# Performance work log

Measured on AMD Instinct MI355X. Metric: run time of the kernel, lower is better.

Reference implementation:

```python
import jax, jax.numpy as jnp
import numpy as np

N_NODES = 100000
EPS = 1e-12  # F.normalize eps


def _sage_conv(x, src, dst, deg, Wl, bl, Wr):
    # mean aggregation of neighbor (source) features at destination nodes
    agg = jax.ops.segment_sum(x[src], dst, num_segments=N_NODES)  # [N, F]
    agg = agg / jnp.maximum(deg, 1.0)[:, None]
    out = agg @ Wl + bl + x @ Wr  # lin_l(mean(x_j)) + lin_r(x_i)
    # normalize=True -> L2 row normalization
    norm = jnp.sqrt(jnp.sum(out * out, axis=-1, keepdims=True))
    return out / jnp.maximum(norm, EPS)


def setup_inputs() -> dict:
    key = jax.random.key(0)
    ks = jax.random.split(key, 10)
    F_IN, H, C = 14, 32, 2
    x = jax.random.normal(ks[0], (N_NODES, F_IN), dtype=jnp.float32)
    edge_index = jax.random.randint(ks[1], (2, 6400000), 0, N_NODES, dtype=jnp.int32)
    def glorot(k, shape):
        lim = float(np.sqrt(6.0 / (shape[0] + shape[1])))
        return jax.random.uniform(k, shape, jnp.float32, -lim, lim)
    return {
        "x": x,
        "edge_index": edge_index,
        "W1l": glorot(ks[2], (F_IN, H)), "b1": jnp.zeros((H,), jnp.float32),
        "W1r": glorot(ks[3], (F_IN, H)),
        "W2l": glorot(ks[4], (H, H)), "b2": jnp.zeros((H,), jnp.float32),
        "W2r": glorot(ks[5], (H, H)),
        "Wlin": glorot(ks[6], (H, C)), "blin": jnp.zeros((C,), jnp.float32),
    }


def reference(x, edge_index, W1l, b1, W1r, W2l, b2, W2r, Wlin, blin):
    src, dst = edge_index[0], edge_index[1]
    deg = jax.ops.segment_sum(jnp.ones_like(dst, dtype=x.dtype), dst,
                              num_segments=N_NODES)  # in-degree per node
    h = jax.nn.relu(_sage_conv(x, src, dst, deg, W1l, b1, W1r))
    # dropout p=0.2 is identity at inference
    h = jax.nn.relu(_sage_conv(h, src, dst, deg, W2l, b2, W2r))
    return h @ Wlin + blin  # [N, num_classes]
```

## Files before the change

### kernel.cpp

```cpp
#include <hip/hip_runtime.h>
#include <hip/hip_bf16.h>


#define CHA 16384
#define MAXB 512
#define CAPB 18432
#define NPB 128

static __device__ __forceinline__ unsigned short f2bf(float f) {
    unsigned u = __float_as_uint(f);
    unsigned r = (u + 0x7FFFu + ((u >> 16) & 1u)) >> 16;
    return (unsigned short)r;
}
#define BF_LO(u) __uint_as_float((u) << 16)
#define BF_HI(u) __uint_as_float((u) & 0xFFFF0000u)

__global__ void cvt_x_bf16(const float* __restrict__ x, unsigned short* __restrict__ xb,
                           int* __restrict__ bcursor, int N, int NB) {
    int idx = blockIdx.x * blockDim.x + threadIdx.x;
    if (idx < NB) bcursor[idx] = idx * CAPB;
    if (idx >= N * 16) return;
    int n = idx >> 4, f = idx & 15;
    float v = (f < 14) ? x[n * 14 + f] : 0.f;
    xb[idx] = f2bf(v);
}

__global__ __launch_bounds__(1024) void partitionA(
        const int* __restrict__ src, const int* __restrict__ dst,
        int* __restrict__ bcursor, unsigned* __restrict__ part, int E, int NB) {
    __shared__ unsigned pk[CHA];
    __shared__ int h[MAXB], lofs[MAXB], cur[MAXB], delta[MAXB], tmp[MAXB];
    int t = threadIdx.x;
    int base = blockIdx.x * CHA;
    int end = base + CHA; if (end > E) end = E;
    int cnt = end - base;

    int ed[16], es[16];
    for (int i = t; i < NB; i += 1024) h[i] = 0;
    __syncthreads();
    #pragma unroll
    for (int i = 0; i < 4; ++i) {
        int j = i * 4096 + t * 4;
        if (j + 4 <= cnt) {
            int4 d4 = *(const int4*)(dst + base + j);
            int4 s4 = *(const int4*)(src + base + j);
            ed[i*4+0] = d4.x; ed[i*4+1] = d4.y; ed[i*4+2] = d4.z; ed[i*4+3] = d4.w;
            es[i*4+0] = s4.x; es[i*4+1] = s4.y; es[i*4+2] = s4.z; es[i*4+3] = s4.w;
            atomicAdd(&h[d4.x >> 8], 1);
            atomicAdd(&h[d4.y >> 8], 1);
            atomicAdd(&h[d4.z >> 8], 1);
            atomicAdd(&h[d4.w >> 8], 1);
        } else {
            #pragma unroll
            for (int k = 0; k < 4; ++k) {
                if (j + k < cnt) {
                    ed[i*4+k] = dst[base + j + k];
                    es[i*4+k] = src[base + j + k];
                    atomicAdd(&h[ed[i*4+k] >> 8], 1);
                } else ed[i*4+k] = -1;
            }
        }
    }
    __syncthreads();
    int v = 0;
    if (t < MAXB) { v = (t < NB) ? h[t] : 0; tmp[t] = v; }
    __syncthreads();
    for (int off = 1; off < MAXB; off <<= 1) {
        int a = 0;
        if (t < MAXB && t >= off) a = tmp[t - off];
        __syncthreads();
        if (t < MAXB) tmp[t] += a;
        __syncthreads();
    }
    if (t < NB) {
        int excl = tmp[t] - v;
        lofs[t] = excl;
        cur[t] = excl;
        int g = v ? atomicAdd(&bcursor[t], v) : 0;
        delta[t] = g - excl;
    }
    __syncthreads();
    #pragma unroll
    for (int i = 0; i < 16; ++i) {
        int d = ed[i];
        if (d >= 0) {
            int b = d >> 8;
            int r = atomicAdd(&cur[b], 1);
            pk[r] = ((unsigned)(d & 255) << 24) | (unsigned)es[i];
        }
    }
    __syncthreads();
    int wid = t >> 6, lane = t & 63;
    for (int b = wid; b < NB; b += 16) {
        int s = lofs[b];
        int e2 = (b + 1 < NB) ? lofs[b + 1] : cnt;
        int dlt = delta[b];
        int lim = (b + 1) * CAPB;
        for (int k = s + lane; k < e2; k += 64) {
            int gidx = dlt + k;
            if (gidx < lim) part[gidx] = pk[k];
        }
    }
}

__global__ __launch_bounds__(1024) void partitionB(
        const unsigned* __restrict__ part, const int* __restrict__ bcursor,
        int* __restrict__ deg, int* __restrict__ offs, int* __restrict__ nlo,
        int* __restrict__ sorted_src, int N, int HALF) {
    __shared__ int pk2[CAPB];
    __shared__ int h[512], tmp[512], keyofs[512];
    int b = blockIdx.x;
    int t = threadIdx.x;
    int start = b * CAPB;
    int end = bcursor[b];
    if (end > start + CAPB) end = start + CAPB;
    int cnt = end - start;
    unsigned ce[18];
    if (t < 512) h[t] = 0;
    __syncthreads();
    #pragma unroll
    for (int i = 0; i < 18; ++i) {
        int idx = start + t + i * 1024;
        unsigned p = 0xFFFFFFFFu;
        if (idx < end) {
            p = part[idx];
            int key = (int)(p >> 24) * 2 + (((int)(p & 0xFFFFFFu) < HALF) ? 0 : 1);
            atomicAdd(&h[key], 1);
        }
        ce[i] = p;
    }
    __syncthreads();
    int v = (t < 512) ? h[t] : 0;
    if (t < 512) tmp[t] = v;
    __syncthreads();
    for (int off = 1; off < 512; off <<= 1) {
        int a = (t < 512 && t >= off) ? tmp[t - off] : 0;
        __syncthreads();
        if (t < 512) tmp[t] += a;
        __syncthreads();
    }
    if (t < 512) keyofs[t] = tmp[t] - v;
    __syncthreads();
    if (t < 256) {
        int lo = h[2 * t];
        int d = lo + h[2 * t + 1];
        int excl = keyofs[2 * t];
        int node = b * 256 + t;
        if (node < N) {
            deg[node] = d;
            offs[node] = start + excl;
            nlo[node] = lo;
        }
    }
    __syncthreads();
    #pragma unroll
    for (int i = 0; i < 18; ++i) {
        unsigned p = ce[i];
        if (p != 0xFFFFFFFFu) {
            int s = (int)(p & 0xFFFFFFu);
            int key = (int)(p >> 24) * 2 + ((s < HALF) ? 0 : 1);
            int r = atomicAdd(&keyofs[key], 1);
            pk2[r] = s;
        }
    }
    __syncthreads();
    for (int i = t; i < cnt; i += 1024)
        sorted_src[start + i] = pk2[i];
}

__global__ void gather14_bf16(const uint4* __restrict__ xb, const int* __restrict__ sorted_src,
                              const int* __restrict__ offs, const int* __restrict__ deg,
                              const int* __restrict__ nlo, float4* __restrict__ agg1,
                              int N, int pass) {
    int idx = blockIdx.x * blockDim.x + threadIdx.x;
    int n = idx >> 1;
    if (n >= N) return;
    int q = idx & 1;
    int start = offs[n];
    int d = deg[n];
    int lo = nlo[n];
    int jbeg = pass ? lo : 0;
    int jend = pass ? d : lo;
    float a0=0,a1=0,a2=0,a3=0,a4=0,a5=0,a6=0,a7=0;
    int j = jbeg;
    for (; j + 4 <= jend; j += 4) {
        int s0 = sorted_src[start + j + 0];
        int s1 = sorted_src[start + j + 1];
        int s2 = sorted_src[start + j + 2];
        int s3 = sorted_src[start + j + 3];
        uint4 u0 = xb[s0 * 2 + q];
        uint4 u1 = xb[s1 * 2 + q];
        uint4 u2 = xb[s2 * 2 + q];
        uint4 u3 = xb[s3 * 2 + q];
        a0 += BF_LO(u0.x) + BF_LO(u1.x) + BF_LO(u2.x) + BF_LO(u3.x);
        a1 += BF_HI(u0.x) + BF_HI(u1.x) + BF_HI(u2.x) + BF_HI(u3.x);
        a2 += BF_LO(u0.y) + BF_LO(u1.y) + BF_LO(u2.y) + BF_LO(u3.y);
        a3 += BF_HI(u0.y) + BF_HI(u1.y) + BF_HI(u2.y) + BF_HI(u3.y);
        a4 += BF_LO(u0.z) + BF_LO(u1.z) + BF_LO(u2.z) + BF_LO(u3.z);
        a5 += BF_HI(u0.z) + BF_HI(u1.z) + BF_HI(u2.z) + BF_HI(u3.z);
        a6 += BF_LO(u0.w) + BF_LO(u1.w) + BF_LO(u2.w) + BF_LO(u3.w);
        a7 += BF_HI(u0.w) + BF_HI(u1.w) + BF_HI(u2.w) + BF_HI(u3.w);
    }
    for (; j < jend; ++j) {
        uint4 u0 = xb[sorted_src[start + j] * 2 + q];
        a0 += BF_LO(u0.x); a1 += BF_HI(u0.x);
        a2 += BF_LO(u0.y); a3 += BF_HI(u0.y);
        a4 += BF_LO(u0.z); a5 += BF_HI(u0.z);
        a6 += BF_LO(u0.w); a7 += BF_HI(u0.w);
    }
    if (pass == 0) {
        agg1[n * 4 + q * 2 + 0] = make_float4(a0, a1, a2, a3);
        agg1[n * 4 + q * 2 + 1] = make_float4(a4, a5, a6, a7);
    } else {
        float inv = 1.0f / ((d > 0) ? (float)d : 1.0f);
        float4 p0 = agg1[n * 4 + q * 2 + 0];
        float4 p1 = agg1[n * 4 + q * 2 + 1];
        agg1[n * 4 + q * 2 + 0] = make_float4((p0.x + a0) * inv, (p0.y + a1) * inv,
                                              (p0.z + a2) * inv, (p0.w + a3) * inv);
        agg1[n * 4 + q * 2 + 1] = make_float4((p1.x + a4) * inv, (p1.y + a5) * inv,
                                              (p1.z + a6) * inv, (p1.w + a7) * inv);
    }
}

__global__ void gather32_bf16(const uint4* __restrict__ hb, const int* __restrict__ sorted_src,
                              const int* __restrict__ offs, const int* __restrict__ deg,
                              const int* __restrict__ nlo, float4* __restrict__ agg2,
                              int N, int pass) {
    int idx = blockIdx.x * blockDim.x + threadIdx.x;
    int n = idx >> 2;
    if (n >= N) return;
    int q = idx & 3;
    int start = offs[n];
    int d = deg[n];
    int lo = nlo[n];
    int jbeg = pass ? lo : 0;
    int jend = pass ? d : lo;
    float a0=0,a1=0,a2=0,a3=0,a4=0,a5=0,a6=0,a7=0;
    int j = jbeg;
    for (; j + 4 <= jend; j += 4) {
        int s0 = sorted_src[start + j + 0];
        int s1 = sorted_src[start + j + 1];
        int s2 = sorted_src[start + j + 2];
        int s3 = sorted_src[start + j + 3];
        uint4 u0 = hb[s0 * 4 + q];
        uint4 u1 = hb[s1 * 4 + q];
        uint4 u2 = hb[s2 * 4 + q];
        uint4 u3 = hb[s3 * 4 + q];
        a0 += BF_LO(u0.x) + BF_LO(u1.x) + BF_LO(u2.x) + BF_LO(u3.x);
        a1 += BF_HI(u0.x) + BF_HI(u1.x) + BF_HI(u2.x) + BF_HI(u3.x);
        a2 += BF_LO(u0.y) + BF_LO(u1.y) + BF_LO(u2.y) + BF_LO(u3.y);
        a3 += BF_HI(u0.y) + BF_HI(u1.y) + BF_HI(u2.y) + BF_HI(u3.y);
        a4 += BF_LO(u0.z) + BF_LO(u1.z) + BF_LO(u2.z) + BF_LO(u3.z);
        a5 += BF_HI(u0.z) + BF_HI(u1.z) + BF_HI(u2.z) + BF_HI(u3.z);
        a6 += BF_LO(u0.w) + BF_LO(u1.w) + BF_LO(u2.w) + BF_LO(u3.w);
        a7 += BF_HI(u0.w) + BF_HI(u1.w) + BF_HI(u2.w) + BF_HI(u3.w);
    }
    for (; j < jend; ++j) {
        uint4 u0 = hb[sorted_src[start + j] * 4 + q];
        a0 += BF_LO(u0.x); a1 += BF_HI(u0.x);
        a2 += BF_LO(u0.y); a3 += BF_HI(u0.y);
        a4 += BF_LO(u0.z); a5 += BF_HI(u0.z);
        a6 += BF_LO(u0.w); a7 += BF_HI(u0.w);
    }
    if (pass == 0) {
        agg2[n * 8 + q * 2 + 0] = make_float4(a0, a1, a2, a3);
        agg2[n * 8 + q * 2 + 1] = make_float4(a4, a5, a6, a7);
    } else {
        float inv = 1.0f / ((d > 0) ? (float)d : 1.0f);
        float4 p0 = agg2[n * 8 + q * 2 + 0];
        float4 p1 = agg2[n * 8 + q * 2 + 1];
        agg2[n * 8 + q * 2 + 0] = make_float4((p0.x + a0) * inv, (p0.y + a1) * inv,
                                              (p0.z + a2) * inv, (p0.w + a3) * inv);
        agg2[n * 8 + q * 2 + 1] = make_float4((p1.x + a4) * inv, (p1.y + a5) * inv,
                                              (p1.z + a6) * inv, (p1.w + a7) * inv);
    }
}

__global__ __launch_bounds__(256) void dense1(
        const float* __restrict__ x, const float* __restrict__ agg,
        const float* __restrict__ W1l, const float* __restrict__ b1,
        const float* __restrict__ W1r, float* __restrict__ h,
        unsigned short* __restrict__ hb, int N) {
    __shared__ float sagg[NPB * 17];
    __shared__ float sx[NPB * 15];
    __shared__ float swl[14 * 32], swr[14 * 32], sb[32];
    int t = threadIdx.x;
    int nb = blockIdx.x * NPB;
    int nn = N - nb; if (nn > NPB) nn = NPB;
    const float4* g4 = (const float4*)(agg + (size_t)nb * 16);
    for (int i = t; i < nn * 4; i += 256) {
        float4 v = g4[i];
        float* d = &sagg[(i >> 2) * 17 + (i & 3) * 4];
        d[0] = v.x; d[1] = v.y; d[2] = v.z; d[3] = v.w;
    }
    const float* gx = x + (size_t)nb * 14;
    for (int i = t; i < nn * 14; i += 256) {
        int row = i / 14;
        sx[row * 15 + (i - row * 14)] = gx[i];
    }
    for (int i = t; i < 448; i += 256) { swl[i] = W1l[i]; swr[i] = W1r[i]; }
    if (t < 32) sb[t] = b1[t];
    __syncthreads();
    int q2 = t & 3;
    int p = t >> 2;
    int l0 = p * 2, l1 = l0 + 1;
    float acc0[8], acc1[8];
    #pragma unroll
    for (int j = 0; j < 8; ++j) { acc0[j] = sb[q2 * 8 + j]; acc1[j] = acc0[j]; }
    #pragma unroll
    for (int k = 0; k < 14; ++k) {
        float a0 = sagg[l0 * 17 + k], a1 = sagg[l1 * 17 + k];
        float x0 = sx[l0 * 15 + k],  x1 = sx[l1 * 15 + k];
        const float4* wl4 = (const float4*)&swl[k * 32 + q2 * 8];
        const float4* wr4 = (const float4*)&swr[k * 32 + q2 * 8];
        float4 wla = wl4[0], wlb = wl4[1], wra = wr4[0], wrb = wr4[1];
        acc0[0] += a0 * wla.x + x0 * wra.x;  acc1[0] += a1 * wla.x + x1 * wra.x;
        acc0[1] += a0 * wla.y + x0 * wra.y;  acc1[1] += a1 * wla.y + x1 * wra.y;
        acc0[2] += a0 * wla.z + x0 * wra.z;  acc1[2] += a1 * wla.z + x1 * wra.z;
        acc0[3] += a0 * wla.w + x0 * wra.w;  acc1[3] += a1 * wla.w + x1 * wra.w;
        acc0[4] += a0 * wlb.x + x0 * wrb.x;  acc1[4] += a1 * wlb.x + x1 * wrb.x;
        acc0[5] += a0 * wlb.y + x0 * wrb.y;  acc1[5] += a1 * wlb.y + x1 * wrb.y;
        acc0[6] += a0 * wlb.z + x0 * wrb.z;  acc1[6] += a1 * wlb.z + x1 * wrb.z;
        acc0[7] += a0 * wlb.w + x0 * wrb.w;  acc1[7] += a1 * wlb.w + x1 * wrb.w;
    }
    float ss0 = 0.f, ss1 = 0.f;
    #pragma unroll
    for (int j = 0; j < 8; ++j) { ss0 += acc0[j] * acc0[j]; ss1 += acc1[j] * acc1[j]; }
    ss0 += __shfl_xor(ss0, 1); ss0 += __shfl_xor(ss0, 2);
    ss1 += __shfl_xor(ss1, 1); ss1 += __shfl_xor(ss1, 2);
    float inv0 = 1.f / fmaxf(sqrtf(ss0), 1e-12f);
    float inv1 = 1.f / fmaxf(sqrtf(ss1), 1e-12f);
    int n0 = nb + l0, n1 = nb + l1;
    if (n0 < N) {
        float hv[8];
        #pragma unroll
        for (int j = 0; j < 8; ++j) hv[j] = fmaxf(acc0[j] * inv0, 0.f);
        float4* ho = (float4*)(h + (size_t)n0 * 32);
        ho[q2 * 2 + 0] = make_float4(hv[0], hv[1], hv[2], hv[3]);
        ho[q2 * 2 + 1] = make_float4(hv[4], hv[5], hv[6], hv[7]);
        uint4 pb;
        pb.x = (unsigned)f2bf(hv[0]) | ((unsigned)f2bf(hv[1]) << 16);
        pb.y = (unsigned)f2bf(hv[2]) | ((unsigned)f2bf(hv[3]) << 16);
        pb.z = (unsigned)f2bf(hv[4]) | ((unsigned)f2bf(hv[5]) << 16);
        pb.w = (unsigned)f2bf(hv[6]) | ((unsigned)f2bf(hv[7]) << 16);
        ((uint4*)(hb + (size_t)n0 * 32))[q2] = pb;
    }
    if (n1 < N) {
        float hv[8];
        #pragma unroll
        for (int j = 0; j < 8; ++j) hv[j] = fmaxf(acc1[j] * inv1, 0.f);
        float4* ho = (float4*)(h + (size_t)n1 * 32);
        ho[q2 * 2 + 0] = make_float4(hv[0], hv[1], hv[2], hv[3]);
        ho[q2 * 2 + 1] = make_float4(hv[4], hv[5], hv[6], hv[7]);
        uint4 pb;
        pb.x = (unsigned)f2bf(hv[0]) | ((unsigned)f2bf(hv[1]) << 16);
        pb.y = (unsigned)f2bf(hv[2]) | ((unsigned)f2bf(hv[3]) << 16);
        pb.z = (unsigned)f2bf(hv[4]) | ((unsigned)f2bf(hv[5]) << 16);
        pb.w = (unsigned)f2bf(hv[6]) | ((unsigned)f2bf(hv[7]) << 16);
        ((uint4*)(hb + (size_t)n1 * 32))[q2] = pb;
    }
}

__global__ __launch_bounds__(256) void dense2(
        const float* __restrict__ h, const float* __restrict__ agg2,
        const float* __restrict__ W2l, const float* __restrict__ b2,
        const float* __restrict__ W2r, const float* __restrict__ Wlin,
        const float* __restrict__ blin, float* __restrict__ out, int N) {
    __shared__ float sa[NPB * 33];
    __shared__ float sh2[NPB * 33];
    __shared__ float swl[32 * 32], swr[32 * 32], swo[64], sb[32], sbo[2];
    int t = threadIdx.x;
    int nb = blockIdx.x * NPB;
    int nn = N - nb; if (nn > NPB) nn = NPB;
    const float4* ga = (const float4*)(agg2 + (size_t)nb * 32);
    const float4* gh = (const float4*)(h + (size_t)nb * 32);
    for (int i = t; i < nn * 8; i += 256) {
        float4 v = ga[i];
        float* d = &sa[(i >> 3) * 33 + (i & 7) * 4];
        d[0] = v.x; d[1] = v.y; d[2] = v.z; d[3] = v.w;
        float4 w = gh[i];
        float* e = &sh2[(i >> 3) * 33 + (i & 7) * 4];
        e[0] = w.x; e[1] = w.y; e[2] = w.z; e[3] = w.w;
    }
    for (int i = t; i < 1024; i += 256) { swl[i] = W2l[i]; swr[i] = W2r[i]; }
    if (t < 64) swo[t] = Wlin[t];
    if (t < 32) sb[t] = b2[t];
    if (t < 2) sbo[t] = blin[t];
    __syncthreads();
    int q2 = t & 3;
    int p = t >> 2;
    int l0 = p * 2, l1 = l0 + 1;
    float acc0[8], acc1[8];
    #pragma unroll
    for (int j = 0; j < 8; ++j) { acc0[j] = sb[q2 * 8 + j]; acc1[j] = acc0[j]; }
    for (int k = 0; k < 32; ++k) {
        float a0 = sa[l0 * 33 + k],  a1 = sa[l1 * 33 + k];
        float h0 = sh2[l0 * 33 + k], h1 = sh2[l1 * 33 + k];
        const float4* wl4 = (const float4*)&swl[k * 32 + q2 * 8];
        const float4* wr4 = (const float4*)&swr[k * 32 + q2 * 8];
        float4 wla = wl4[0], wlb = wl4[1], wra = wr4[0], wrb = wr4[1];
        acc0[0] += a0 * wla.x + h0 * wra.x;  acc1[0] += a1 * wla.x + h1 * wra.x;
        acc0[1] += a0 * wla.y + h0 * wra.y;  acc1[1] += a1 * wla.y + h1 * wra.y;
        acc0[2] += a0 * wla.z + h0 * wra.z;  acc1[2] += a1 * wla.z + h1 * wra.z;
        acc0[3] += a0 * wla.w + h0 * wra.w;  acc1[3] += a1 * wla.w + h1 * wra.w;
        acc0[4] += a0 * wlb.x + h0 * wrb.x;  acc1[4] += a1 * wlb.x + h1 * wrb.x;
        acc0[5] += a0 * wlb.y + h0 * wrb.y;  acc1[5] += a1 * wlb.y + h1 * wrb.y;
        acc0[6] += a0 * wlb.z + h0 * wrb.z;  acc1[6] += a1 * wlb.z + h1 * wrb.z;
        acc0[7] += a0 * wlb.w + h0 * wrb.w;  acc1[7] += a1 * wlb.w + h1 * wrb.w;
    }
    float ss0 = 0.f, ss1 = 0.f;
    #pragma unroll
    for (int j = 0; j < 8; ++j) { ss0 += acc0[j] * acc0[j]; ss1 += acc1[j] * acc1[j]; }
    ss0 += __shfl_xor(ss0, 1); ss0 += __shfl_xor(ss0, 2);
    ss1 += __shfl_xor(ss1, 1); ss1 += __shfl_xor(ss1, 2);
    float inv0 = 1.f / fmaxf(sqrtf(ss0), 1e-12f);
    float inv1 = 1.f / fmaxf(sqrtf(ss1), 1e-12f);
    float o00 = 0.f, o01 = 0.f, o10 = 0.f, o11 = 0.f;
    #pragma unroll
    for (int j = 0; j < 8; ++j) {
        float hv0 = fmaxf(acc0[j] * inv0, 0.f);
        float hv1 = fmaxf(acc1[j] * inv1, 0.f);
        int kk = q2 * 8 + j;
        o00 += hv0 * swo[kk * 2 + 0];
        o01 += hv0 * swo[kk * 2 + 1];
        o10 += hv1 * swo[kk * 2 + 0];
        o11 += hv1 * swo[kk * 2 + 1];
    }
    o00 += __shfl_xor(o00, 1); o00 += __shfl_xor(o00, 2);
    o01 += __shfl_xor(o01, 1); o01 += __shfl_xor(o01, 2);
    o10 += __shfl_xor(o10, 1); o10 += __shfl_xor(o10, 2);
    o11 += __shfl_xor(o11, 1); o11 += __shfl_xor(o11, 2);
    if (q2 == 0) {
        int n0 = nb + l0, n1 = nb + l1;
        if (n0 < N) { out[n0 * 2 + 0] = o00 + sbo[0]; out[n0 * 2 + 1] = o01 + sbo[1]; }
        if (n1 < N) { out[n1 * 2 + 0] = o10 + sbo[0]; out[n1 * 2 + 1] = o11 + sbo[1]; }
    }
}

extern "C" void kernel_launch(void* const* d_in, const int* in_sizes, int n_in,
                              void* d_out, int out_size, void* d_ws, size_t ws_size,
                              hipStream_t stream) {
    const float* x    = (const float*)d_in[0];
    const int*   ei   = (const int*)d_in[1];
    const float* W1l  = (const float*)d_in[2];
    const float* b1   = (const float*)d_in[3];
    const float* W1r  = (const float*)d_in[4];
    const float* W2l  = (const float*)d_in[5];
    const float* b2   = (const float*)d_in[6];
    const float* W2r  = (const float*)d_in[7];
    const float* Wlin = (const float*)d_in[8];
    const float* blin = (const float*)d_in[9];
    float* out = (float*)d_out;

    const int N = in_sizes[0] / 14;
    const int E = in_sizes[1] / 2;
    const int* src = ei;
    const int* dst = ei + E;
    const int NB = (N + 255) / 256;
    const int HALF = N / 2;

    char* ws = (char*)d_ws;
    size_t off = 0;
    auto alloc = [&](size_t bytes) -> void* {
        void* p = ws + off;
        off = (off + bytes + 255) & ~(size_t)255;
        return p;
    };
    int*            bcursor    = (int*)alloc((size_t)NB * 4);
    unsigned*       part       = (unsigned*)alloc((size_t)NB * CAPB * 4);
    int*            sorted_src = (int*)alloc((size_t)NB * CAPB * 4);
    int*            deg        = (int*)alloc((size_t)N * 4);
    int*            offs       = (int*)alloc((size_t)N * 4);
    int*            nlo        = (int*)alloc((size_t)N * 4);
    unsigned short* xb         = (unsigned short*)alloc((size_t)N * 16 * 2);
    float*          agg1       = (float*)alloc((size_t)N * 16 * 4);
    float*          hbuf       = (float*)alloc((size_t)N * 32 * 4);
    unsigned short* hb         = (unsigned short*)alloc((size_t)N * 32 * 2);
    float*          agg2       = (float*)part;
    (void)ws_size; (void)n_in; (void)out_size;

    cvt_x_bf16<<<(N * 16 + 255) / 256, 256, 0, stream>>>(x, xb, bcursor, N, NB);
    partitionA<<<(E + CHA - 1) / CHA, 1024, 0, stream>>>(src, dst, bcursor, part, E, NB);
    partitionB<<<NB, 1024, 0, stream>>>(part, bcursor, deg, offs, nlo, sorted_src, N, HALF);

    const int DB = (N + NPB - 1) / NPB;
    gather14_bf16<<<(N * 2 + 255) / 256, 256, 0, stream>>>(
        (const uint4*)xb, sorted_src, offs, deg, nlo, (float4*)agg1, N, 0);
    gather14_bf16<<<(N * 2 + 255) / 256, 256, 0, stream>>>(
        (const uint4*)xb, sorted_src, offs, deg, nlo, (float4*)agg1, N, 1);
    dense1<<<DB, 256, 0, stream>>>(x, agg1, W1l, b1, W1r, hbuf, hb, N);
    gather32_bf16<<<(N * 4 + 255) / 256, 256, 0, stream>>>(
        (const uint4*)hb, sorted_src, offs, deg, nlo, (float4*)agg2, N, 0);
    gather32_bf16<<<(N * 4 + 255) / 256, 256, 0, stream>>>(
        (const uint4*)hb, sorted_src, offs, deg, nlo, (float4*)agg2, N, 1);
    dense2<<<DB, 256, 0, stream>>>(hbuf, agg2, W2l, b2, W2r, Wlin, blin, out, N);
}
```

Baseline: 295.4 us.

## Fuse layer-1 gather and dense into partition kernel; fuse layer-2 pass1 with dense2

Layer-1 aggregation now runs inside the per-bucket partition kernel, reading neighbor indices straight from shared memory, then applies the first dense layer, normalization and bf16 packing before writing h. The second pass of the layer-2 gather is merged with dense2, so each thread computes partial 32-wide products and reduces them with shuffles. This drops the agg1 buffer and four separate launches along with their global round trips. In exchange, the partition kernel uses more shared memory and registers, which can lower occupancy, and dense2 keeps 32 accumulators per thread.

```diff
diff --git a/kernel.cpp b/kernel.cpp
--- a/kernel.cpp
+++ b/kernel.cpp
@@ -5,7 +5,6 @@
 #define CHA 16384
 #define MAXB 512
 #define CAPB 18432
-#define NPB 128
 
 static __device__ __forceinline__ unsigned short f2bf(float f) {
     unsigned u = __float_as_uint(f);
@@ -103,12 +102,20 @@
     }
 }
 
-__global__ __launch_bounds__(1024) void partitionB(
+__global__ __launch_bounds__(1024) void partitionB_fused(
         const unsigned* __restrict__ part, const int* __restrict__ bcursor,
+        const uint4* __restrict__ xb4, const float* __restrict__ x,
+        const float* __restrict__ W1l, const float* __restrict__ b1,
+        const float* __restrict__ W1r,
         int* __restrict__ deg, int* __restrict__ offs, int* __restrict__ nlo,
-        int* __restrict__ sorted_src, int N, int HALF) {
+        int* __restrict__ sorted_src, float* __restrict__ hbuf,
+        unsigned short* __restrict__ hb, int N, int HALF) {
     __shared__ int pk2[CAPB];
-    __shared__ int h[512], tmp[512], keyofs[512];
+    __shared__ int hh[512], tmp[512], keyofs[512];
+    __shared__ int lstart[256], ldeg[256];
+    __shared__ float sagg[256 * 17];
+    __shared__ float sx[256 * 14];
+    __shared__ float swl[448], swr[448], sb1[32];
     int b = blockIdx.x;
     int t = threadIdx.x;
     int start = b * CAPB;
@@ -116,7 +123,9 @@
     if (end > start + CAPB) end = start + CAPB;
     int cnt = end - start;
     unsigned ce[18];
-    if (t < 512) h[t] = 0;
+    if (t < 512) hh[t] = 0;
+    if (t < 448) { swl[t] = W1l[t]; swr[t] = W1r[t]; }
+    else if (t < 480) sb1[t - 448] = b1[t - 448];
     __syncthreads();
     #pragma unroll
     for (int i = 0; i < 18; ++i) {
@@ -125,26 +134,33 @@
         if (idx < end) {
             p = part[idx];
             int key = (int)(p >> 24) * 2 + (((int)(p & 0xFFFFFFu) < HALF) ? 0 : 1);
-            atomicAdd(&h[key], 1);
+            atomicAdd(&hh[key], 1);
         }
         ce[i] = p;
     }
-    __syncthreads();
-    int v = (t < 512) ? h[t] : 0;
+    {
+        int nnod = N - b * 256; if (nnod > 256) nnod = 256; if (nnod < 0) nnod = 0;
+        const float* gx = x + (size_t)b * 256 * 14;
+        for (int i = t; i < nnod * 14; i += 1024) sx[i] = gx[i];
+    }
+    __syncthreads();
+    int v = (t < 512) ? hh[t] : 0;
     if (t < 512) tmp[t] = v;
     __syncthreads();
     for (int off = 1; off < 512; off <<= 1) {
-        int a = (t < 512 && t >= off) ? tmp[t - off] : 0;
+        int a2 = (t < 512 && t >= off) ? tmp[t - off] : 0;
         __syncthreads();
-        if (t < 512) tmp[t] += a;
+        if (t < 512) tmp[t] += a2;
         __syncthreads();
     }
     if (t < 512) keyofs[t] = tmp[t] - v;
     __syncthreads();
     if (t < 256) {
-        int lo = h[2 * t];
-        int d = lo + h[2 * t + 1];
+        int lo = hh[2 * t];
+        int d = lo + hh[2 * t + 1];
         int excl = keyofs[2 * t];
+        lstart[t] = excl;
+        ldeg[t] = d;
         int node = b * 256 + t;
         if (node < N) {
             deg[node] = d;
@@ -166,77 +182,92 @@
     __syncthreads();
     for (int i = t; i < cnt; i += 1024)
         sorted_src[start + i] = pk2[i];
-}
-
-__global__ void gather14_bf16(const uint4* __restrict__ xb, const int* __restrict__ sorted_src,
-                              const int* __restrict__ offs, const int* __restrict__ deg,
-                              const int* __restrict__ nlo, float4* __restrict__ agg1,
-                              int N, int pass) {
-    int idx = blockIdx.x * blockDim.x + threadIdx.x;
-    int n = idx >> 1;
-    if (n >= N) return;
-    int q = idx & 1;
-    int start = offs[n];
-    int d = deg[n];
-    int lo = nlo[n];
-    int jbeg = pass ? lo : 0;
-    int jend = pass ? d : lo;
-    float a0=0,a1=0,a2=0,a3=0,a4=0,a5=0,a6=0,a7=0;
-    int j = jbeg;
-    for (; j + 4 <= jend; j += 4) {
-        int s0 = sorted_src[start + j + 0];
-        int s1 = sorted_src[start + j + 1];
-        int s2 = sorted_src[start + j + 2];
-        int s3 = sorted_src[start + j + 3];
-        uint4 u0 = xb[s0 * 2 + q];
-        uint4 u1 = xb[s1 * 2 + q];
-        uint4 u2 = xb[s2 * 2 + q];
-        uint4 u3 = xb[s3 * 2 + q];
-        a0 += BF_LO(u0.x) + BF_LO(u1.x) + BF_LO(u2.x) + BF_LO(u3.x);
-        a1 += BF_HI(u0.x) + BF_HI(u1.x) + BF_HI(u2.x) + BF_HI(u3.x);
-        a2 += BF_LO(u0.y) + BF_LO(u1.y) + BF_LO(u2.y) + BF_LO(u3.y);
-        a3 += BF_HI(u0.y) + BF_HI(u1.y) + BF_HI(u2.y) + BF_HI(u3.y);
-        a4 += BF_LO(u0.z) + BF_LO(u1.z) + BF_LO(u2.z) + BF_LO(u3.z);
-        a5 += BF_HI(u0.z) + BF_HI(u1.z) + BF_HI(u2.z) + BF_HI(u3.z);
-        a6 += BF_LO(u0.w) + BF_LO(u1.w) + BF_LO(u2.w) + BF_LO(u3.w);
-        a7 += BF_HI(u0.w) + BF_HI(u1.w) + BF_HI(u2.w) + BF_HI(u3.w);
-    }
-    for (; j < jend; ++j) {
-        uint4 u0 = xb[sorted_src[start + j] * 2 + q];
-        a0 += BF_LO(u0.x); a1 += BF_HI(u0.x);
-        a2 += BF_LO(u0.y); a3 += BF_HI(u0.y);
-        a4 += BF_LO(u0.z); a5 += BF_HI(u0.z);
-        a6 += BF_LO(u0.w); a7 += BF_HI(u0.w);
-    }
-    if (pass == 0) {
-        agg1[n * 4 + q * 2 + 0] = make_float4(a0, a1, a2, a3);
-        agg1[n * 4 + q * 2 + 1] = make_float4(a4, a5, a6, a7);
-    } else {
-        float inv = 1.0f / ((d > 0) ? (float)d : 1.0f);
-        float4 p0 = agg1[n * 4 + q * 2 + 0];
-        float4 p1 = agg1[n * 4 + q * 2 + 1];
-        agg1[n * 4 + q * 2 + 0] = make_float4((p0.x + a0) * inv, (p0.y + a1) * inv,
-                                              (p0.z + a2) * inv, (p0.w + a3) * inv);
-        agg1[n * 4 + q * 2 + 1] = make_float4((p1.x + a4) * inv, (p1.y + a5) * inv,
-                                              (p1.z + a6) * inv, (p1.w + a7) * inv);
-    }
-}
-
-__global__ void gather32_bf16(const uint4* __restrict__ hb, const int* __restrict__ sorted_src,
-                              const int* __restrict__ offs, const int* __restrict__ deg,
-                              const int* __restrict__ nlo, float4* __restrict__ agg2,
-                              int N, int pass) {
+
+    int node = t >> 2, sub = t & 3, ep = sub >> 1, half = sub & 1;
+    int js = lstart[node], d = ldeg[node];
+    int je = js + d;
+    float a[8] = {0,0,0,0,0,0,0,0};
+    int j = js + ep;
+    for (; j + 6 < je; j += 8) {
+        int s0 = pk2[j], s1 = pk2[j+2], s2 = pk2[j+4], s3 = pk2[j+6];
+        uint4 u0 = xb4[s0*2+half], u1 = xb4[s1*2+half], u2 = xb4[s2*2+half], u3 = xb4[s3*2+half];
+        a[0] += BF_LO(u0.x)+BF_LO(u1.x)+BF_LO(u2.x)+BF_LO(u3.x);
+        a[1] += BF_HI(u0.x)+BF_HI(u1.x)+BF_HI(u2.x)+BF_HI(u3.x);
+        a[2] += BF_LO(u0.y)+BF_LO(u1.y)+BF_LO(u2.y)+BF_LO(u3.y);
+        a[3] += BF_HI(u0.y)+BF_HI(u1.y)+BF_HI(u2.y)+BF_HI(u3.y);
+        a[4] += BF_LO(u0.z)+BF_LO(u1.z)+BF_LO(u2.z)+BF_LO(u3.z);
+        a[5] += BF_HI(u0.z)+BF_HI(u1.z)+BF_HI(u2.z)+BF_HI(u3.z);
+        a[6] += BF_LO(u0.w)+BF_LO(u1.w)+BF_LO(u2.w)+BF_LO(u3.w);
+        a[7] += BF_HI(u0.w)+BF_HI(u1.w)+BF_HI(u2.w)+BF_HI(u3.w);
+    }
+    for (; j < je; j += 2) {
+        uint4 u0 = xb4[pk2[j]*2+half];
+        a[0] += BF_LO(u0.x); a[1] += BF_HI(u0.x);
+        a[2] += BF_LO(u0.y); a[3] += BF_HI(u0.y);
+        a[4] += BF_LO(u0.z); a[5] += BF_HI(u0.z);
+        a[6] += BF_LO(u0.w); a[7] += BF_HI(u0.w);
+    }
+    #pragma unroll
+    for (int i = 0; i < 8; ++i) a[i] += __shfl_xor(a[i], 2);
+    if (ep == 0) {
+        #pragma unroll
+        for (int i = 0; i < 8; ++i) sagg[node * 17 + half * 8 + i] = a[i];
+    }
+    __syncthreads();
+
+    float inv = 1.0f / ((d > 0) ? (float)d : 1.0f);
+    float acc[8];
+    #pragma unroll
+    for (int i = 0; i < 8; ++i) acc[i] = sb1[sub * 8 + i];
+    #pragma unroll
+    for (int k = 0; k < 14; ++k) {
+        float ag = sagg[node * 17 + k] * inv;
+        float xv = sx[node * 14 + k];
+        const float4* wl4 = (const float4*)&swl[k * 32 + sub * 8];
+        const float4* wr4 = (const float4*)&swr[k * 32 + sub * 8];
+        float4 wla = wl4[0], wlb = wl4[1], wra = wr4[0], wrb = wr4[1];
+        acc[0] += ag * wla.x + xv * wra.x;
+        acc[1] += ag * wla.y + xv * wra.y;
+        acc[2] += ag * wla.z + xv * wra.z;
+        acc[3] += ag * wla.w + xv * wra.w;
+        acc[4] += ag * wlb.x + xv * wrb.x;
+        acc[5] += ag * wlb.y + xv * wrb.y;
+        acc[6] += ag * wlb.z + xv * wrb.z;
+        acc[7] += ag * wlb.w + xv * wrb.w;
+    }
+    float ss = 0.f;
+    #pragma unroll
+    for (int i = 0; i < 8; ++i) ss += acc[i] * acc[i];
+    ss += __shfl_xor(ss, 1); ss += __shfl_xor(ss, 2);
+    float invn = 1.f / fmaxf(sqrtf(ss), 1e-12f);
+    int gnode = b * 256 + node;
+    if (gnode < N) {
+        float hv[8];
+        #pragma unroll
+        for (int i = 0; i < 8; ++i) hv[i] = fmaxf(acc[i] * invn, 0.f);
+        float4* ho = (float4*)(hbuf + (size_t)gnode * 32 + sub * 8);
+        ho[0] = make_float4(hv[0], hv[1], hv[2], hv[3]);
+        ho[1] = make_float4(hv[4], hv[5], hv[6], hv[7]);
+        uint4 pb;
+        pb.x = (unsigned)f2bf(hv[0]) | ((unsigned)f2bf(hv[1]) << 16);
+        pb.y = (unsigned)f2bf(hv[2]) | ((unsigned)f2bf(hv[3]) << 16);
+        pb.z = (unsigned)f2bf(hv[4]) | ((unsigned)f2bf(hv[5]) << 16);
+        pb.w = (unsigned)f2bf(hv[6]) | ((unsigned)f2bf(hv[7]) << 16);
+        *(uint4*)(hb + (size_t)gnode * 32 + sub * 8) = pb;
+    }
+}
+
+__global__ void gather32_p0(const uint4* __restrict__ hb, const int* __restrict__ sorted_src,
+                            const int* __restrict__ offs, const int* __restrict__ nlo,
+                            float4* __restrict__ agg2, int N) {
     int idx = blockIdx.x * blockDim.x + threadIdx.x;
     int n = idx >> 2;
     if (n >= N) return;
     int q = idx & 3;
     int start = offs[n];
-    int d = deg[n];
-    int lo = nlo[n];
-    int jbeg = pass ? lo : 0;
-    int jend = pass ? d : lo;
+    int jend = nlo[n];
     float a0=0,a1=0,a2=0,a3=0,a4=0,a5=0,a6=0,a7=0;
-    int j = jbeg;
+    int j = 0;
     for (; j + 4 <= jend; j += 4) {
         int s0 = sorted_src[start + j + 0];
         int s1 = sorted_src[start + j + 1];
@@ -262,178 +293,119 @@
         a4 += BF_LO(u0.z); a5 += BF_HI(u0.z);
         a6 += BF_LO(u0.w); a7 += BF_HI(u0.w);
     }
-    if (pass == 0) {
-        agg2[n * 8 + q * 2 + 0] = make_float4(a0, a1, a2, a3);
-        agg2[n * 8 + q * 2 + 1] = make_float4(a4, a5, a6, a7);
-    } else {
-        float inv = 1.0f / ((d > 0) ? (float)d : 1.0f);
-        float4 p0 = agg2[n * 8 + q * 2 + 0];
-        float4 p1 = agg2[n * 8 + q * 2 + 1];
-        agg2[n * 8 + q * 2 + 0] = make_float4((p0.x + a0) * inv, (p0.y + a1) * inv,
-                                              (p0.z + a2) * inv, (p0.w + a3) * inv);
-        agg2[n * 8 + q * 2 + 1] = make_float4((p1.x + a4) * inv, (p1.y + a5) * inv,
-                                              (p1.z + a6) * inv, (p1.w + a7) * inv);
-    }
-}
-
-__global__ __launch_bounds__(256) void dense1(
-        const float* __restrict__ x, const float* __restrict__ agg,
-        const float* __restrict__ W1l, const float* __restrict__ b1,
-        const float* __restrict__ W1r, float* __restrict__ h,
-        unsigned short* __restrict__ hb, int N) {
-    __shared__ float sagg[NPB * 17];
-    __shared__ float sx[NPB * 15];
-    __shared__ float swl[14 * 32], swr[14 * 32], sb[32];
-    int t = threadIdx.x;
-    int nb = blockIdx.x * NPB;
-    int nn = N - nb; if (nn > NPB) nn = NPB;
-    const float4* g4 = (const float4*)(agg + (size_t)nb * 16);
-    for (int i = t; i < nn * 4; i += 256) {
-        float4 v = g4[i];
-        float* d = &sagg[(i >> 2) * 17 + (i & 3) * 4];
-        d[0] = v.x; d[1] = v.y; d[2] = v.z; d[3] = v.w;
-    }
-    const float* gx = x + (size_t)nb * 14;
-    for (int i = t; i < nn * 14; i += 256) {
-        int row = i / 14;
-        sx[row * 15 + (i - row * 14)] = gx[i];
-    }
-    for (int i = t; i < 448; i += 256) { swl[i] = W1l[i]; swr[i] = W1r[i]; }
-    if (t < 32) sb[t] = b1[t];
-    __syncthreads();
-    int q2 = t & 3;
-    int p = t >> 2;
-    int l0 = p * 2, l1 = l0 + 1;
-    float acc0[8], acc1[8];
-    #pragma unroll
-    for (int j = 0; j < 8; ++j) { acc0[j] = sb[q2 * 8 + j]; acc1[j] = acc0[j]; }
-    #pragma unroll
-    for (int k = 0; k < 14; ++k) {
-        float a0 = sagg[l0 * 17 + k], a1 = sagg[l1 * 17 + k];
-        float x0 = sx[l0 * 15 + k],  x1 = sx[l1 * 15 + k];
-        const float4* wl4 = (const float4*)&swl[k * 32 + q2 * 8];
-        const float4* wr4 = (const float4*)&swr[k * 32 + q2 * 8];
-        float4 wla = wl4[0], wlb = wl4[1], wra = wr4[0], wrb = wr4[1];
-        acc0[0] += a0 * wla.x + x0 * wra.x;  acc1[0] += a1 * wla.x + x1 * wra.x;
-        acc0[1] += a0 * wla.y + x0 * wra.y;  acc1[1] += a1 * wla.y + x1 * wra.y;
-        acc0[2] += a0 * wla.z + x0 * wra.z;  acc1[2] += a1 * wla.z + x1 * wra.z;
-        acc0[3] += a0 * wla.w + x0 * wra.w;  acc1[3] += a1 * wla.w + x1 * wra.w;
-        acc0[4] += a0 * wlb.x + x0 * wrb.x;  acc1[4] += a1 * wlb.x + x1 * wrb.x;
-        acc0[5] += a0 * wlb.y + x0 * wrb.y;  acc1[5] += a1 * wlb.y + x1 * wrb.y;
-        acc0[6] += a0 * wlb.z + x0 * wrb.z;  acc1[6] += a1 * wlb.z + x1 * wrb.z;
-        acc0[7] += a0 * wlb.w + x0 * wrb.w;  acc1[7] += a1 * wlb.w + x1 * wrb.w;
-    }
-    float ss0 = 0.f, ss1 = 0.f;
-    #pragma unroll
-    for (int j = 0; j < 8; ++j) { ss0 += acc0[j] * acc0[j]; ss1 += acc1[j] * acc1[j]; }
-    ss0 += __shfl_xor(ss0, 1); ss0 += __shfl_xor(ss0, 2);
-    ss1 += __shfl_xor(ss1, 1); ss1 += __shfl_xor(ss1, 2);
-    float inv0 = 1.f / fmaxf(sqrtf(ss0), 1e-12f);
-    float inv1 = 1.f / fmaxf(sqrtf(ss1), 1e-12f);
-    int n0 = nb + l0, n1 = nb + l1;
-    if (n0 < N) {
-        float hv[8];
-        #pragma unroll
-        for (int j = 0; j < 8; ++j) hv[j] = fmaxf(acc0[j] * inv0, 0.f);
-        float4* ho = (float4*)(h + (size_t)n0 * 32);
-        ho[q2 * 2 + 0] = make_float4(hv[0], hv[1], hv[2], hv[3]);
-        ho[q2 * 2 + 1] = make_float4(hv[4], hv[5], hv[6], hv[7]);
-        uint4 pb;
-        pb.x = (unsigned)f2bf(hv[0]) | ((unsigned)f2bf(hv[1]) << 16);
-        pb.y = (unsigned)f2bf(hv[2]) | ((unsigned)f2bf(hv[3]) << 16);
-        pb.z = (unsigned)f2bf(hv[4]) | ((unsigned)f2bf(hv[5]) << 16);
-        pb.w = (unsigned)f2bf(hv[6]) | ((unsigned)f2bf(hv[7]) << 16);
-        ((uint4*)(hb + (size_t)n0 * 32))[q2] = pb;
-    }
-    if (n1 < N) {
-        float hv[8];
-        #pragma unroll
-        for (int j = 0; j < 8; ++j) hv[j] = fmaxf(acc1[j] * inv1, 0.f);
-        float4* ho = (float4*)(h + (size_t)n1 * 32);
-        ho[q2 * 2 + 0] = make_float4(hv[0], hv[1], hv[2], hv[3]);
-        ho[q2 * 2 + 1] = make_float4(hv[4], hv[5], hv[6], hv[7]);
-        uint4 pb;
-        pb.x = (unsigned)f2bf(hv[0]) | ((unsigned)f2bf(hv[1]) << 16);
-        pb.y = (unsigned)f2bf(hv[2]) | ((unsigned)f2bf(hv[3]) << 16);
-        pb.z = (unsigned)f2bf(hv[4]) | ((unsigned)f2bf(hv[5]) << 16);
-        pb.w = (unsigned)f2bf(hv[6]) | ((unsigned)f2bf(hv[7]) << 16);
-        ((uint4*)(hb + (size_t)n1 * 32))[q2] = pb;
-    }
-}
-
-__global__ __launch_bounds__(256) void dense2(
-        const float* __restrict__ h, const float* __restrict__ agg2,
+    agg2[n * 8 + q * 2 + 0] = make_float4(a0, a1, a2, a3);
+    agg2[n * 8 + q * 2 + 1] = make_float4(a4, a5, a6, a7);
+}
+
+__global__ __launch_bounds__(256) void g32p1_dense2(
+        const uint4* __restrict__ hb4, const int* __restrict__ sorted_src,
+        const int* __restrict__ offs, const int* __restrict__ deg,
+        const int* __restrict__ nlo, const float* __restrict__ agg2p,
+        const float* __restrict__ hbuf,
         const float* __restrict__ W2l, const float* __restrict__ b2,
         const float* __restrict__ W2r, const float* __restrict__ Wlin,
         const float* __restrict__ blin, float* __restrict__ out, int N) {
-    __shared__ float sa[NPB * 33];
-    __shared__ float sh2[NPB * 33];
-    __shared__ float swl[32 * 32], swr[32 * 32], swo[64], sb[32], sbo[2];
+    __shared__ float swl[1024], swr[1024], swo[64], sb2[32], sbo[2];
     int t = threadIdx.x;
-    int nb = blockIdx.x * NPB;
-    int nn = N - nb; if (nn > NPB) nn = NPB;
-    const float4* ga = (const float4*)(agg2 + (size_t)nb * 32);
-    const float4* gh = (const float4*)(h + (size_t)nb * 32);
-    for (int i = t; i < nn * 8; i += 256) {
-        float4 v = ga[i];
-        float* d = &sa[(i >> 3) * 33 + (i & 7) * 4];
-        d[0] = v.x; d[1] = v.y; d[2] = v.z; d[3] = v.w;
-        float4 w = gh[i];
-        float* e = &sh2[(i >> 3) * 33 + (i & 7) * 4];
-        e[0] = w.x; e[1] = w.y; e[2] = w.z; e[3] = w.w;
-    }
     for (int i = t; i < 1024; i += 256) { swl[i] = W2l[i]; swr[i] = W2r[i]; }
     if (t < 64) swo[t] = Wlin[t];
-    if (t < 32) sb[t] = b2[t];
+    if (t < 32) sb2[t] = b2[t];
     if (t < 2) sbo[t] = blin[t];
     __syncthreads();
-    int q2 = t & 3;
-    int p = t >> 2;
-    int l0 = p * 2, l1 = l0 + 1;
-    float acc0[8], acc1[8];
-    #pragma unroll
-    for (int j = 0; j < 8; ++j) { acc0[j] = sb[q2 * 8 + j]; acc1[j] = acc0[j]; }
-    for (int k = 0; k < 32; ++k) {
-        float a0 = sa[l0 * 33 + k],  a1 = sa[l1 * 33 + k];
-        float h0 = sh2[l0 * 33 + k], h1 = sh2[l1 * 33 + k];
-        const float4* wl4 = (const float4*)&swl[k * 32 + q2 * 8];
-        const float4* wr4 = (const float4*)&swr[k * 32 + q2 * 8];
-        float4 wla = wl4[0], wlb = wl4[1], wra = wr4[0], wrb = wr4[1];
-        acc0[0] += a0 * wla.x + h0 * wra.x;  acc1[0] += a1 * wla.x + h1 * wra.x;
-        acc0[1] += a0 * wla.y + h0 * wra.y;  acc1[1] += a1 * wla.y + h1 * wra.y;
-        acc0[2] += a0 * wla.z + h0 * wra.z;  acc1[2] += a1 * wla.z + h1 * wra.z;
-        acc0[3] += a0 * wla.w + h0 * wra.w;  acc1[3] += a1 * wla.w + h1 * wra.w;
-        acc0[4] += a0 * wlb.x + h0 * wrb.x;  acc1[4] += a1 * wlb.x + h1 * wrb.x;
-        acc0[5] += a0 * wlb.y + h0 * wrb.y;  acc1[5] += a1 * wlb.y + h1 * wrb.y;
-        acc0[6] += a0 * wlb.z + h0 * wrb.z;  acc1[6] += a1 * wlb.z + h1 * wrb.z;
-        acc0[7] += a0 * wlb.w + h0 * wrb.w;  acc1[7] += a1 * wlb.w + h1 * wrb.w;
-    }
-    float ss0 = 0.f, ss1 = 0.f;
-    #pragma unroll
-    for (int j = 0; j < 8; ++j) { ss0 += acc0[j] * acc0[j]; ss1 += acc1[j] * acc1[j]; }
-    ss0 += __shfl_xor(ss0, 1); ss0 += __shfl_xor(ss0, 2);
-    ss1 += __shfl_xor(ss1, 1); ss1 += __shfl_xor(ss1, 2);
-    float inv0 = 1.f / fmaxf(sqrtf(ss0), 1e-12f);
-    float inv1 = 1.f / fmaxf(sqrtf(ss1), 1e-12f);
-    float o00 = 0.f, o01 = 0.f, o10 = 0.f, o11 = 0.f;
-    #pragma unroll
-    for (int j = 0; j < 8; ++j) {
-        float hv0 = fmaxf(acc0[j] * inv0, 0.f);
-        float hv1 = fmaxf(acc1[j] * inv1, 0.f);
-        int kk = q2 * 8 + j;
-        o00 += hv0 * swo[kk * 2 + 0];
-        o01 += hv0 * swo[kk * 2 + 1];
-        o10 += hv1 * swo[kk * 2 + 0];
-        o11 += hv1 * swo[kk * 2 + 1];
-    }
-    o00 += __shfl_xor(o00, 1); o00 += __shfl_xor(o00, 2);
-    o01 += __shfl_xor(o01, 1); o01 += __shfl_xor(o01, 2);
-    o10 += __shfl_xor(o10, 1); o10 += __shfl_xor(o10, 2);
-    o11 += __shfl_xor(o11, 1); o11 += __shfl_xor(o11, 2);
-    if (q2 == 0) {
-        int n0 = nb + l0, n1 = nb + l1;
-        if (n0 < N) { out[n0 * 2 + 0] = o00 + sbo[0]; out[n0 * 2 + 1] = o01 + sbo[1]; }
-        if (n1 < N) { out[n1 * 2 + 0] = o10 + sbo[0]; out[n1 * 2 + 1] = o11 + sbo[1]; }
+    int idx = blockIdx.x * 256 + t;
+    int n = idx >> 2;
+    if (n >= N) return;
+    int q = idx & 3;
+    int start = offs[n], d = deg[n], lo = nlo[n];
+    float a[8] = {0,0,0,0,0,0,0,0};
+    int j = lo;
+    for (; j + 4 <= d; j += 4) {
+        int s0 = sorted_src[start + j + 0];
+        int s1 = sorted_src[start + j + 1];
+        int s2 = sorted_src[start + j + 2];
+        int s3 = sorted_src[start + j + 3];
+        uint4 u0 = hb4[s0 * 4 + q];
+        uint4 u1 = hb4[s1 * 4 + q];
+        uint4 u2 = hb4[s2 * 4 + q];
+        uint4 u3 = hb4[s3 * 4 + q];
+        a[0] += BF_LO(u0.x)+BF_LO(u1.x)+BF_LO(u2.x)+BF_LO(u3.x);
+        a[1] += BF_HI(u0.x)+BF_HI(u1.x)+BF_HI(u2.x)+BF_HI(u3.x);
+        a[2] += BF_LO(u0.y)+BF_LO(u1.y)+BF_LO(u2.y)+BF_LO(u3.y);
+        a[3] += BF_HI(u0.y)+BF_HI(u1.y)+BF_HI(u2.y)+BF_HI(u3.y);
+        a[4] += BF_LO(u0.z)+BF_LO(u1.z)+BF_LO(u2.z)+BF_LO(u3.z);
+        a[5] += BF_HI(u0.z)+BF_HI(u1.z)+BF_HI(u2.z)+BF_HI(u3.z);
+        a[6] += BF_LO(u0.w)+BF_LO(u1.w)+BF_LO(u2.w)+BF_LO(u3.w);
+        a[7] += BF_HI(u0.w)+BF_HI(u1.w)+BF_HI(u2.w)+BF_HI(u3.w);
+    }
+    for (; j < d; ++j) {
+        uint4 u0 = hb4[sorted_src[start + j] * 4 + q];
+        a[0] += BF_LO(u0.x); a[1] += BF_HI(u0.x);
+        a[2] += BF_LO(u0.y); a[3] += BF_HI(u0.y);
+        a[4] += BF_LO(u0.z); a[5] += BF_HI(u0.z);
+        a[6] += BF_LO(u0.w); a[7] += BF_HI(u0.w);
+    }
+    float inv = 1.0f / ((d > 0) ? (float)d : 1.0f);
+    const float4* gp = (const float4*)(agg2p + (size_t)n * 32 + q * 8);
+    float4 p0 = gp[0], p1 = gp[1];
+    float av[8];
+    av[0] = (p0.x + a[0]) * inv; av[1] = (p0.y + a[1]) * inv;
+    av[2] = (p0.z + a[2]) * inv; av[3] = (p0.w + a[3]) * inv;
+    av[4] = (p1.x + a[4]) * inv; av[5] = (p1.y + a[5]) * inv;
+    av[6] = (p1.z + a[6]) * inv; av[7] = (p1.w + a[7]) * inv;
+    const float4* gh = (const float4*)(hbuf + (size_t)n * 32 + q * 8);
+    float4 h0 = gh[0], h1 = gh[1];
+    float hv8[8] = {h0.x, h0.y, h0.z, h0.w, h1.x, h1.y, h1.z, h1.w};
+    float p[32];
+    #pragma unroll
+    for (int o = 0; o < 32; ++o) p[o] = 0.f;
+    #pragma unroll
+    for (int k = 0; k < 8; ++k) {
+        int kk = q * 8 + k;
+        const float4* wl4 = (const float4*)&swl[kk * 32];
+        const float4* wr4 = (const float4*)&swr[kk * 32];
+        #pragma unroll
+        for (int o4 = 0; o4 < 8; ++o4) {
+            float4 wl = wl4[o4], wr = wr4[o4];
+            p[o4*4+0] += av[k] * wl.x + hv8[k] * wr.x;
+            p[o4*4+1] += av[k] * wl.y + hv8[k] * wr.y;
+            p[o4*4+2] += av[k] * wl.z + hv8[k] * wr.z;
+            p[o4*4+3] += av[k] * wl.w + hv8[k] * wr.w;
+        }
+    }
+    bool hi2 = (q & 2) != 0;
+    float keep16[16];
+    #pragma unroll
+    for (int i = 0; i < 16; ++i) {
+        float kv = hi2 ? p[i + 16] : p[i];
+        float sv = hi2 ? p[i] : p[i + 16];
+        keep16[i] = kv + __shfl_xor(sv, 2);
+    }
+    bool hi1 = (q & 1) != 0;
+    float lin[8];
+    #pragma unroll
+    for (int i = 0; i < 8; ++i) {
+        float kv = hi1 ? keep16[i + 8] : keep16[i];
+        float sv = hi1 ? keep16[i] : keep16[i + 8];
+        lin[i] = kv + __shfl_xor(sv, 1) + sb2[q * 8 + i];
+    }
+    float ss = 0.f;
+    #pragma unroll
+    for (int i = 0; i < 8; ++i) ss += lin[i] * lin[i];
+    ss += __shfl_xor(ss, 1); ss += __shfl_xor(ss, 2);
+    float invn = 1.f / fmaxf(sqrtf(ss), 1e-12f);
+    float o0 = 0.f, o1 = 0.f;
+    #pragma unroll
+    for (int i = 0; i < 8; ++i) {
+        float hv = fmaxf(lin[i] * invn, 0.f);
+        int kk = q * 8 + i;
+        o0 += hv * swo[kk * 2 + 0];
+        o1 += hv * swo[kk * 2 + 1];
+    }
+    o0 += __shfl_xor(o0, 1); o0 += __shfl_xor(o0, 2);
+    o1 += __shfl_xor(o1, 1); o1 += __shfl_xor(o1, 2);
+    if (q == 0) {
+        out[n * 2 + 0] = o0 + sbo[0];
+        out[n * 2 + 1] = o1 + sbo[1];
     }
 }
 
@@ -473,7 +445,6 @@
     int*            offs       = (int*)alloc((size_t)N * 4);
     int*            nlo        = (int*)alloc((size_t)N * 4);
     unsigned short* xb         = (unsigned short*)alloc((size_t)N * 16 * 2);
-    float*          agg1       = (float*)alloc((size_t)N * 16 * 4);
     float*          hbuf       = (float*)alloc((size_t)N * 32 * 4);
     unsigned short* hb         = (unsigned short*)alloc((size_t)N * 32 * 2);
     float*          agg2       = (float*)part;
@@ -481,17 +452,12 @@
 
     cvt_x_bf16<<<(N * 16 + 255) / 256, 256, 0, stream>>>(x, xb, bcursor, N, NB);
     partitionA<<<(E + CHA - 1) / CHA, 1024, 0, stream>>>(src, dst, bcursor, part, E, NB);
-    partitionB<<<NB, 1024, 0, stream>>>(part, bcursor, deg, offs, nlo, sorted_src, N, HALF);
-
-    const int DB = (N + NPB - 1) / NPB;
-    gather14_bf16<<<(N * 2 + 255) / 256, 256, 0, stream>>>(
-        (const uint4*)xb, sorted_src, offs, deg, nlo, (float4*)agg1, N, 0);
-    gather14_bf16<<<(N * 2 + 255) / 256, 256, 0, stream>>>(
-        (const uint4*)xb, sorted_src, offs, deg, nlo, (float4*)agg1, N, 1);
-    dense1<<<DB, 256, 0, stream>>>(x, agg1, W1l, b1, W1r, hbuf, hb, N);
-    gather32_bf16<<<(N * 4 + 255) / 256, 256, 0, stream>>>(
-        (const uint4*)hb, sorted_src, offs, deg, nlo, (float4*)agg2, N, 0);
-    gather32_bf16<<<(N * 4 + 255) / 256, 256, 0, stream>>>(
-        (const uint4*)hb, sorted_src, offs, deg, nlo, (float4*)agg2, N, 1);
-    dense2<<<DB, 256, 0, stream>>>(hbuf, agg2, W2l, b2, W2r, Wlin, blin, out, N);
-}
+    partitionB_fused<<<NB, 1024, 0, stream>>>(
+        part, bcursor, (const uint4*)xb, x, W1l, b1, W1r,
+        deg, offs, nlo, sorted_src, hbuf, hb, N, HALF);
+    gather32_p0<<<(N * 4 + 255) / 256, 256, 0, stream>>>(
+        (const uint4*)hb, sorted_src, offs, nlo, (float4*)agg2, N);
+    g32p1_dense2<<<(N * 4 + 255) / 256, 256, 0, stream>>>(
+        (const uint4*)hb, sorted_src, offs, deg, nlo, agg2, hbuf,
+        W2l, b2, W2r, Wlin, blin, out, N);
+}
```

New measurement: 298.6 us. Within noise of the previous version (+1.1%).
